# Optimization experiments

Hardware: AMD Instinct MI355X
Metric: run time of the kernel (lower is better)

## Reference

```python
import jax, jax.numpy as jnp
from jax import lax
import numpy as np

N_PARTICLES = 100000  # number of emitters (state.shape[0])
N_FRAMES = 500


def setup_inputs() -> dict:
    key = jax.random.key(0)
    # one-hot initial state over 2 photophysical states (on/off)
    idx = jax.random.randint(key, (N_PARTICLES,), 0, 2)
    initial = jax.nn.one_hot(idx, 2, dtype=jnp.float32)
    # transition_matrix[0] = identity (stay), transition_matrix[1] = swap (switch)
    transition_matrix = jnp.array(
        [[[1.0, 0.0], [0.0, 1.0]], [[0.0, 1.0], [1.0, 0.0]]], dtype=jnp.float32
    )
    # transition[1][1] from init; chosen so p = initial_trans * randint(1,10) stays in (0,1)
    initial_trans = jnp.array([0.05], dtype=jnp.float32)
    return {
        "initial": initial,
        "transition_matrix": transition_matrix,
        "initial_trans": initial_trans,
        "n_frames": N_FRAMES,
    }


def reference(initial, transition_matrix, initial_trans, n_frames):
    # initial: [N, 2] one-hot float; transition_matrix: [2, 2, 2]; initial_trans: [1]
    N = initial.shape[0]
    base = jax.random.key(42)

    def step(carry, i):
        state, p = carry
        k = jax.random.fold_in(base, i)
        ku, kr = jax.random.split(k)
        # every 100 frames: refresh switching probability p = initial_trans * randint(1, 10)
        r = jax.random.randint(kr, (), 1, 10).astype(jnp.float32)
        p = jnp.where(i % 100 == 0, initial_trans[0] * r, p)
        # Categorical([[0.5, 0.5], [1-p, p]]).sample([N]) -> A in {0,1}^{N,2}
        # row 0 samples 1 w.p. 0.5, row 1 samples 1 w.p. p
        u = jax.random.uniform(ku, (N, 2), dtype=jnp.float32)
        probs1 = jnp.stack([jnp.float32(0.5), p])  # [2] prob of drawing category 1
        A = (u < probs1[None, :]).astype(jnp.float32)  # [N, 2]
        # t = sum(state * A, -1): picks the sample for each particle's current state
        t = jnp.sum(state * A, axis=-1).astype(jnp.int32)  # [N]
        m = transition_matrix[t]  # [N, 2, 2]: identity or swap
        state = jnp.einsum('nc,ncd->nd', state, m)  # [N, 2]
        # original appends np.where(state[:,0]==1)[0]; we return the equivalent
        # fixed-shape indicator state[:, 0] per frame (jit-compatible)
        return (state, p), state[:, 0]

    (_, _), chain = lax.scan(step, (initial, initial_trans[0]), jnp.arange(n_frames))
    return chain  # [n_frames, N]
```

## Files before the change

### kernel.cpp

```cpp
#include <hip/hip_runtime.h>
#include <stdint.h>

__device__ __forceinline__ void tf2x32(uint32_t k0, uint32_t k1,
                                       uint32_t x0, uint32_t x1,
                                       uint32_t& o0, uint32_t& o1) {
  const uint32_t ks2 = k0 ^ k1 ^ 0x1BD11BDAu;
  x0 += k0; x1 += k1;
#define TF_R(r) { x0 += x1; x1 = __builtin_rotateleft32(x1, (r)); x1 ^= x0; }
  TF_R(13) TF_R(15) TF_R(26) TF_R(6)
  x0 += k1; x1 += ks2 + 1u;
  TF_R(17) TF_R(29) TF_R(16) TF_R(24)
  x0 += ks2; x1 += k0 + 2u;
  TF_R(13) TF_R(15) TF_R(26) TF_R(6)
  x0 += k0; x1 += k1 + 3u;
  TF_R(17) TF_R(29) TF_R(16) TF_R(24)
  x0 += k1; x1 += ks2 + 4u;
  TF_R(13) TF_R(15) TF_R(26) TF_R(6)
  x0 += ks2; x1 += k0 + 5u;
#undef TF_R
  o0 = x0; o1 = x1;
}

#define LCHUNK 100
#define F0     8

__global__ __launch_bounds__(256) void hmm_sched(
    const float* __restrict__ initial_trans,
    uint4* __restrict__ sched, int nf) {
  const int gi = blockIdx.x * blockDim.x + threadIdx.x;
  if (gi >= nf) return;
  const float trans = initial_trans[0];
  uint32_t f0_, f1_, t0, t1;
  tf2x32(0u, 42u, 0u, (uint32_t)gi, f0_, f1_);
  tf2x32(f0_, f1_, 0u, 0u, t0, t1);
  const int jf = gi - (gi % 100);
  uint32_t g0, g1, kr0, kr1, a0, a1, b0, b1, h0, h1, l0, l1;
  tf2x32(0u, 42u, 0u, (uint32_t)jf, g0, g1);
  tf2x32(g0, g1, 0u, 1u, kr0, kr1);
  tf2x32(kr0, kr1, 0u, 0u, a0, a1);
  tf2x32(kr0, kr1, 0u, 1u, b0, b1);
  tf2x32(a0, a1, 0u, 0u, h0, h1);
  tf2x32(b0, b1, 0u, 0u, l0, l1);
  const uint32_t hb = h0 ^ h1, lb = l0 ^ l1;
  const uint32_t off = ((hb % 9u) * 4u + (lb % 9u)) % 9u;
  const float p = trans * (float)(1u + off);
  const uint32_t mant = (uint32_t)ceilf(p * 8388608.0f);
  sched[gi] = make_uint4(t0, t1, mant << 9, 0u);
}

__device__ __forceinline__ uint32_t bothstep(uint32_t k0, uint32_t k1,
                                             uint32_t tp, uint32_t twon,
                                             uint32_t& sA, uint32_t& sB) {
  uint32_t a0, a1, b0, b1;
  tf2x32(k0, k1, 0u, twon, a0, a1);
  tf2x32(k0, k1, 0u, twon + 1u, b0, b1);
  const uint32_t flip0 = ((a0 ^ a1) < 0x80000000u) ? 1u : 0u;
  const uint32_t flip1 = ((b0 ^ b1) < tp) ? 1u : 0u;
  sA = sA ? (1u ^ flip1) : flip0;
  sB = sB ? (1u ^ flip1) : flip0;
  return (sA != sB) ? 1u : 0u;
}

__device__ __forceinline__ void mstep(uint32_t k0, uint32_t k1, uint32_t tp,
                                      uint32_t twon, uint32_t& s) {
  uint32_t a0, a1;
  tf2x32(k0, k1, 0u, twon + s, a0, a1);
  const uint32_t thr = s ? tp : 0x80000000u;
  s ^= ((a0 ^ a1) < thr) ? 1u : 0u;
}

__global__ __launch_bounds__(256) void hmm_main(
    const float* __restrict__ initial,
    const uint4* __restrict__ sched,
    float* __restrict__ out,
    uint32_t* __restrict__ fin,
    int N, int nf) {
  const int t = blockIdx.x * blockDim.x + threadIdx.x;
  const int n0 = 2 * t;
  if (n0 >= N) return;
  const int c = blockIdx.y;
  const int c0 = c * LCHUNK;
  const int Leff = min(LCHUNK, nf - c0);
  if (Leff <= 0) return;

  const uint4* __restrict__ sch = sched + c0;
  const uint32_t twon0 = 2u * (uint32_t)n0;
  const uint32_t twon1 = twon0 + 2u;
  float2* o = (float2*)(out + (size_t)c0 * N + n0);
  const int ostr = N >> 1;

  uint32_t s0A, s0B, s1A, s1B, mf0 = 0, mf1 = 0;
  int f = 0;

  if (c == 0) {
    const float4 iv = *(const float4*)(initial + 2 * n0);
    s0A = (iv.x < 0.5f) ? 1u : 0u;  s0B = s0A;
    s1A = (iv.z < 0.5f) ? 1u : 0u;  s1B = s1A;
  } else {
    s0A = 0u; s0B = 1u; s1A = 0u; s1B = 1u;
    uint32_t d = 1u;
    for (; f < Leff; ++f) {
      if (f >= F0 && !__any((int)d)) break;
      const uint4 sc = sch[f];
      const uint32_t d0 = bothstep(sc.x, sc.y, sc.z, twon0, s0A, s0B);
      const uint32_t d1 = bothstep(sc.x, sc.y, sc.z, twon1, s1A, s1B);
      mf0 += d0; mf1 += d1; d = d0 | d1;
      *o = make_float2(s0A ? 0.0f : 1.0f, s1A ? 0.0f : 1.0f);
      o += ostr;
    }
  }
  const int fm = f;
  for (; f < Leff; ++f) {
    const uint4 sc = sch[f];
    mstep(sc.x, sc.y, sc.z, twon0, s0A);
    mstep(sc.x, sc.y, sc.z, twon1, s1A);
    *o = make_float2(s0A ? 0.0f : 1.0f, s1A ? 0.0f : 1.0f);
    o += ostr;
  }
  if (fm < Leff) { s0B = s0A; s1B = s1A; }
  *(uint2*)(fin + (size_t)c * N + n0) =
      make_uint2(s0A | (s0B << 1) | (mf0 << 2), s1A | (s1B << 1) | (mf1 << 2));
}

__global__ __launch_bounds__(256) void hmm_fix(
    const float* __restrict__ initial,
    float* __restrict__ out,
    const uint32_t* __restrict__ fin,
    int N, int C) {
  const int n = blockIdx.x * blockDim.x + threadIdx.x;
  if (n >= N) return;
  uint32_t s = (initial[2 * n] < 0.5f) ? 1u : 0u;
  for (int c = 0; c < C; ++c) {
    const uint32_t w = fin[(size_t)c * N + n];
    if (c > 0 && s == 1u) {
      const int c0 = c * LCHUNK;
      const int mf = (int)(w >> 2);
      for (int f = 0; f < mf; ++f) {
        float* q = out + (size_t)(c0 + f) * N + n;
        *q = 1.0f - *q;
      }
    }
    s = (s == 0u) ? (w & 1u) : ((w >> 1) & 1u);
  }
}

extern "C" void kernel_launch(void* const* d_in, const int* in_sizes, int n_in,
                              void* d_out, int out_size, void* d_ws, size_t ws_size,
                              hipStream_t stream) {
  const float* initial = (const float*)d_in[0];
  const float* initial_trans = (const float*)d_in[2];
  float* out = (float*)d_out;

  const int N = in_sizes[0] / 2;
  const int nf = out_size / N;
  const int C = (nf + LCHUNK - 1) / LCHUNK;

  uint4* sched = (uint4*)d_ws;
  const size_t finoff = (((size_t)nf * 16) + 511) & ~(size_t)511;
  uint32_t* fin = (uint32_t*)((char*)d_ws + finoff);

  hipLaunchKernelGGL(hmm_sched, dim3((nf + 255) / 256), dim3(256), 0, stream,
                     initial_trans, sched, nf);
  const int gx = (N / 2 + 255) / 256;
  hipLaunchKernelGGL(hmm_main, dim3(gx, C), dim3(256), 0, stream,
                     initial, sched, out, fin, N, nf);
  hipLaunchKernelGGL(hmm_fix, dim3((N + 255) / 256), dim3(256), 0, stream,
                     initial, out, fin, N, C);
}
```

Measured before the change: 135.6 us.

## Process four particles per thread, halve chunk length, pack chunk summaries into bytes

Each thread now advances four particles instead of two and stores a float4 per frame. The frame chunk length drops from 100 to 50, so twice as many chunks run in parallel in the grid-y dimension. Per-chunk summaries are packed into one byte per particle, which is valid because the mismatch count now fits in six bits. The schedule entry for the next frame is prefetched one iteration ahead, and one extra schedule entry is generated so that prefetch stays in bounds. The aim is more instruction-level parallelism, wider stores and less summary traffic, at the cost of more chunk boundaries needing the two-hypothesis warm-up and more fix-up work.

```diff
diff --git a/kernel.cpp b/kernel.cpp
--- a/kernel.cpp
+++ b/kernel.cpp
@@ -21,14 +21,14 @@
   o0 = x0; o1 = x1;
 }
 
-#define LCHUNK 100
+#define LCHUNK 50
 #define F0     8
 
 __global__ __launch_bounds__(256) void hmm_sched(
     const float* __restrict__ initial_trans,
     uint4* __restrict__ sched, int nf) {
   const int gi = blockIdx.x * blockDim.x + threadIdx.x;
-  if (gi >= nf) return;
+  if (gi > nf) return;
   const float trans = initial_trans[0];
   uint32_t f0_, f1_, t0, t1;
   tf2x32(0u, 42u, 0u, (uint32_t)gi, f0_, f1_);
@@ -73,10 +73,10 @@
     const float* __restrict__ initial,
     const uint4* __restrict__ sched,
     float* __restrict__ out,
-    uint32_t* __restrict__ fin,
+    uchar4* __restrict__ fin,
     int N, int nf) {
   const int t = blockIdx.x * blockDim.x + threadIdx.x;
-  const int n0 = 2 * t;
+  const int n0 = 4 * t;
   if (n0 >= N) return;
   const int c = blockIdx.y;
   const int c0 = c * LCHUNK;
@@ -84,48 +84,68 @@
   if (Leff <= 0) return;
 
   const uint4* __restrict__ sch = sched + c0;
-  const uint32_t twon0 = 2u * (uint32_t)n0;
-  const uint32_t twon1 = twon0 + 2u;
-  float2* o = (float2*)(out + (size_t)c0 * N + n0);
-  const int ostr = N >> 1;
+  const uint32_t base = 8u * (uint32_t)t;
+  float4* o = (float4*)(out + (size_t)c0 * N + n0);
+  const int ostr = N >> 2;
 
-  uint32_t s0A, s0B, s1A, s1B, mf0 = 0, mf1 = 0;
+  uint32_t sA[4], sB[4], mf[4] = {0u, 0u, 0u, 0u};
   int f = 0;
 
   if (c == 0) {
-    const float4 iv = *(const float4*)(initial + 2 * n0);
-    s0A = (iv.x < 0.5f) ? 1u : 0u;  s0B = s0A;
-    s1A = (iv.z < 0.5f) ? 1u : 0u;  s1B = s1A;
+    const float4 iv0 = ((const float4*)initial)[2 * t];
+    const float4 iv1 = ((const float4*)initial)[2 * t + 1];
+    sA[0] = (iv0.x < 0.5f) ? 1u : 0u;
+    sA[1] = (iv0.z < 0.5f) ? 1u : 0u;
+    sA[2] = (iv1.x < 0.5f) ? 1u : 0u;
+    sA[3] = (iv1.z < 0.5f) ? 1u : 0u;
+#pragma unroll
+    for (int i = 0; i < 4; ++i) sB[i] = sA[i];
   } else {
-    s0A = 0u; s0B = 1u; s1A = 0u; s1B = 1u;
+#pragma unroll
+    for (int i = 0; i < 4; ++i) { sA[i] = 0u; sB[i] = 1u; }
     uint32_t d = 1u;
     for (; f < Leff; ++f) {
       if (f >= F0 && !__any((int)d)) break;
       const uint4 sc = sch[f];
-      const uint32_t d0 = bothstep(sc.x, sc.y, sc.z, twon0, s0A, s0B);
-      const uint32_t d1 = bothstep(sc.x, sc.y, sc.z, twon1, s1A, s1B);
-      mf0 += d0; mf1 += d1; d = d0 | d1;
-      *o = make_float2(s0A ? 0.0f : 1.0f, s1A ? 0.0f : 1.0f);
+      d = 0u;
+#pragma unroll
+      for (int i = 0; i < 4; ++i) {
+        const uint32_t di =
+            bothstep(sc.x, sc.y, sc.z, base + 2u * i, sA[i], sB[i]);
+        mf[i] += di; d |= di;
+      }
+      *o = make_float4(sA[0] ? 0.0f : 1.0f, sA[1] ? 0.0f : 1.0f,
+                       sA[2] ? 0.0f : 1.0f, sA[3] ? 0.0f : 1.0f);
       o += ostr;
     }
   }
   const int fm = f;
+  uint4 sc = sch[f < Leff ? f : Leff - 1];
   for (; f < Leff; ++f) {
-    const uint4 sc = sch[f];
-    mstep(sc.x, sc.y, sc.z, twon0, s0A);
-    mstep(sc.x, sc.y, sc.z, twon1, s1A);
-    *o = make_float2(s0A ? 0.0f : 1.0f, s1A ? 0.0f : 1.0f);
+    const uint4 scn = sch[f + 1];
+#pragma unroll
+    for (int i = 0; i < 4; ++i) mstep(sc.x, sc.y, sc.z, base + 2u * i, sA[i]);
+    *o = make_float4(sA[0] ? 0.0f : 1.0f, sA[1] ? 0.0f : 1.0f,
+                     sA[2] ? 0.0f : 1.0f, sA[3] ? 0.0f : 1.0f);
     o += ostr;
+    sc = scn;
   }
-  if (fm < Leff) { s0B = s0A; s1B = s1A; }
-  *(uint2*)(fin + (size_t)c * N + n0) =
-      make_uint2(s0A | (s0B << 1) | (mf0 << 2), s1A | (s1B << 1) | (mf1 << 2));
+  if (fm < Leff) {
+#pragma unroll
+    for (int i = 0; i < 4; ++i) sB[i] = sA[i];
+  }
+  uchar4 w;
+  w.x = (uint8_t)(sA[0] | (sB[0] << 1) | (mf[0] << 2));
+  w.y = (uint8_t)(sA[1] | (sB[1] << 1) | (mf[1] << 2));
+  w.z = (uint8_t)(sA[2] | (sB[2] << 1) | (mf[2] << 2));
+  w.w = (uint8_t)(sA[3] | (sB[3] << 1) | (mf[3] << 2));
+  fin[(size_t)c * (N >> 2) + t] = w;
 }
 
 __global__ __launch_bounds__(256) void hmm_fix(
     const float* __restrict__ initial,
     float* __restrict__ out,
-    const uint32_t* __restrict__ fin,
+    const uint8_t* __restrict__ fin,
     int N, int C) {
   const int n = blockIdx.x * blockDim.x + threadIdx.x;
   if (n >= N) return;
@@ -156,14 +176,14 @@
   const int C = (nf + LCHUNK - 1) / LCHUNK;
 
   uint4* sched = (uint4*)d_ws;
-  const size_t finoff = (((size_t)nf * 16) + 511) & ~(size_t)511;
-  uint32_t* fin = (uint32_t*)((char*)d_ws + finoff);
+  const size_t finoff = (((size_t)(nf + 1) * 16) + 511) & ~(size_t)511;
+  uint8_t* fin = (uint8_t*)d_ws + finoff;
 
-  hipLaunchKernelGGL(hmm_sched, dim3((nf + 255) / 256), dim3(256), 0, stream,
+  hipLaunchKernelGGL(hmm_sched, dim3((nf + 1 + 255) / 256), dim3(256), 0, stream,
                      initial_trans, sched, nf);
-  const int gx = (N / 2 + 255) / 256;
+  const int gx = (N / 4 + 255) / 256;
   hipLaunchKernelGGL(hmm_main, dim3(gx, C), dim3(256), 0, stream,
-                     initial, sched, out, fin, N, nf);
+                     initial, sched, out, (uchar4*)fin, N, nf);
   hipLaunchKernelGGL(hmm_fix, dim3((N + 255) / 256), dim3(256), 0, stream,
                      initial, out, fin, N, C);
 }
```

New measurement: 158.3 us. 1.17x slower.
